# Kernel optimization log

Measured on AMD Instinct MI355X. Metric: run time of the kernel, lower is better.

The kernel has to match this reference:

```python
import jax, jax.numpy as jnp
import numpy as np

N_NODES = 100000
N_EDGES = 1600000
D_IN = 128
D_HID = 64
N_CLASSES = 64


def setup_inputs() -> dict:
    key = jax.random.key(0)
    ks = jax.random.split(key, 12)
    x = jax.random.normal(ks[0], (N_NODES, D_IN), dtype=jnp.float32)
    edge_index = jax.random.randint(ks[1], (2, N_EDGES), 0, N_NODES, dtype=jnp.int64)
    def lin(k, fan_in, fan_out):
        k1, k2 = jax.random.split(k)
        bound = 1.0 / np.sqrt(fan_in)
        w = jax.random.uniform(k1, (fan_in, fan_out), jnp.float32, -bound, bound)
        b = jax.random.uniform(k2, (fan_out,), jnp.float32, -bound, bound)
        return w, b
    w1a, b1a = lin(ks[2], D_IN, D_HID)
    w1b, b1b = lin(ks[3], D_HID, D_HID)
    w2a, b2a = lin(ks[4], D_HID, D_HID)
    w2b, b2b = lin(ks[5], D_HID, N_CLASSES)
    return {"x": x, "edge_index": edge_index,
            "w1a": w1a, "b1a": b1a, "w1b": w1b, "b1b": b1b,
            "w2a": w2a, "b2a": b2a, "w2b": w2b, "b2b": b2b}


def _gin_agg(x, src, dst):
    # GINConv with eps=0: (1+eps)*x_i + sum_{j->i} x_j
    agg = jax.ops.segment_sum(x[src], dst, num_segments=N_NODES)
    return x + agg


def reference(x, edge_index, w1a, b1a, w1b, b1b, w2a, b2a, w2b, b2b):
    src, dst = edge_index[0], edge_index[1]
    # conv1: MLP = Linear -> ReLU -> Linear -> ReLU
    h = _gin_agg(x, src, dst)
    h = jax.nn.relu(h @ w1a + b1a)
    h = jax.nn.relu(h @ w1b + b1b)
    # conv2: MLP = Linear -> ReLU -> Linear
    h = _gin_agg(h, src, dst)
    h = jax.nn.relu(h @ w2a + b2a)
    h = h @ w2b + b2b
    # global add pool over the single graph -> [1, num_classes]
    return jnp.sum(h, axis=0, keepdims=True)
```

## Files before the change

kernel.cpp:

```cpp
#include <hip/hip_runtime.h>

#define N_NODES 100000
#define N_EDGES 1600000
#define D_IN 128
#define D 64

#define NBLK 1000
#define EPB  1600
#define NB2  391
#define SC_M  (NB2 * NBLK)
#define SC_CH 1024
#define SC_NB ((SC_M + SC_CH - 1) / SC_CH)

__device__ __forceinline__ float bf2f(unsigned short u) {
    union { unsigned int i; float f; } q; q.i = ((unsigned int)u) << 16; return q.f;
}
__device__ __forceinline__ unsigned short f2bf(float f) {
    unsigned int u = __float_as_uint(f);
    unsigned int r = (u + 0x7FFFu + ((u >> 16) & 1u)) >> 16;
    return (unsigned short)r;
}
__device__ __forceinline__ void acc4(float4& a, ushort4 v) {
    a.x += bf2f(v.x); a.y += bf2f(v.y); a.z += bf2f(v.z); a.w += bf2f(v.w);
}


__global__ __launch_bounds__(256) void k_hist1(const int* __restrict__ dst,
                                               int* __restrict__ bh) {
    __shared__ int h[NB2];
    int t = threadIdx.x;
    for (int i = t; i < NB2; i += 256) h[i] = 0;
    __syncthreads();
    int base = blockIdx.x * EPB;
    for (int i = t; i < EPB; i += 256) atomicAdd(&h[dst[base + i] >> 8], 1);
    __syncthreads();
    for (int i = t; i < NB2; i += 256) bh[i * NBLK + blockIdx.x] = h[i];
}

__global__ __launch_bounds__(256) void k_scanA(const int* __restrict__ bh,
                                               int* __restrict__ part) {
    __shared__ int s[256];
    int t = threadIdx.x;
    int base = blockIdx.x * SC_CH + t * 4;
    int sum = 0;
    if (base + 3 < SC_M) {
        int4 v = *(const int4*)(bh + base);
        sum = (v.x + v.y) + (v.z + v.w);
    } else {
        for (int k = 0; k < 4; k++) if (base + k < SC_M) sum += bh[base + k];
    }
    s[t] = sum;
    __syncthreads();
    for (int o = 128; o > 0; o >>= 1) {
        if (t < o) s[t] += s[t + o];
        __syncthreads();
    }
    if (t == 0) part[blockIdx.x] = s[0];
}

__global__ __launch_bounds__(512) void k_scanB(int* __restrict__ part) {
    __shared__ int s[512];
    int t = threadIdx.x;
    int v = (t < SC_NB) ? part[t] : 0;
    s[t] = v;
    __syncthreads();
    for (int o = 1; o < 512; o <<= 1) {
        int x = (t >= o) ? s[t - o] : 0;
        __syncthreads();
        s[t] += x;
        __syncthreads();
    }
    if (t < SC_NB) part[t] = s[t] - v;
}

__global__ __launch_bounds__(256) void k_scanC(int* __restrict__ bh,
                                               const int* __restrict__ part) {
    __shared__ int s[256];
    int t = threadIdx.x;
    int base = blockIdx.x * SC_CH + t * 4;
    int4 v = {0, 0, 0, 0};
    if (base + 3 < SC_M) v = *(const int4*)(bh + base);
    else { for (int k = 0; k < 4; k++) if (base + k < SC_M) (&v.x)[k] = bh[base + k]; }
    int sum = (v.x + v.y) + (v.z + v.w);
    s[t] = sum;
    __syncthreads();
    for (int o = 1; o < 256; o <<= 1) {
        int x = (t >= o) ? s[t - o] : 0;
        __syncthreads();
        s[t] += x;
        __syncthreads();
    }
    int run = part[blockIdx.x] + s[t] - sum;
    int4 w;
    w.x = run; run += v.x;
    w.y = run; run += v.y;
    w.z = run; run += v.z;
    w.w = run;
    if (base + 3 < SC_M) *(int4*)(bh + base) = w;
    else { for (int k = 0; k < 4; k++) if (base + k < SC_M) bh[base + k] = (&w.x)[k]; }
}

__global__ __launch_bounds__(256) void k_scatter1(const int* __restrict__ src,
                                                  const int* __restrict__ dst,
                                                  const int* __restrict__ bh,
                                                  uint2* __restrict__ tmp) {
    __shared__ int cur[NB2];
    int t = threadIdx.x;
    for (int i = t; i < NB2; i += 256) cur[i] = bh[i * NBLK + blockIdx.x];
    __syncthreads();
    int base = blockIdx.x * EPB;
    for (int i = t; i < EPB; i += 256) {
        int d = dst[base + i];
        int sv = src[base + i];
        int p = atomicAdd(&cur[d >> 8], 1);
        tmp[p] = make_uint2((unsigned)d, (unsigned)sv);
    }
}

__global__ __launch_bounds__(256) void k_build(const uint2* __restrict__ tmp,
                                               const int* __restrict__ bh,
                                               int* __restrict__ offs,
                                               int* __restrict__ csr) {
    __shared__ int deg[256];
    __shared__ int s[256];
    __shared__ int cur[256];
    int b = blockIdx.x;
    int t = threadIdx.x;
    int e0 = bh[b * NBLK];
    int e1 = (b == NB2 - 1) ? N_EDGES : bh[(b + 1) * NBLK];
    deg[t] = 0;
    __syncthreads();
    for (int i = e0 + t; i < e1; i += 256) atomicAdd(&deg[tmp[i].x & 255u], 1);
    __syncthreads();
    int v = deg[t];
    s[t] = v;
    __syncthreads();
    for (int o = 1; o < 256; o <<= 1) {
        int x = (t >= o) ? s[t - o] : 0;
        __syncthreads();
        s[t] += x;
        __syncthreads();
    }
    int start = e0 + s[t] - v;
    int node = b * 256 + t;
    if (node < N_NODES) offs[node] = start;
    cur[t] = start;
    __syncthreads();
    for (int i = e0 + t; i < e1; i += 256) {
        uint2 p = tmp[i];
        int pos = atomicAdd(&cur[p.x & 255u], 1);
        csr[pos] = (int)p.y;
    }
    if (b == 0 && t == 0) offs[N_NODES] = N_EDGES;
}

__global__ __launch_bounds__(256) void k_gemm1(const float* __restrict__ x,
                                               const float* __restrict__ w,
                                               unsigned short* __restrict__ z) {
    __shared__ float ws[D_IN][D];
    __shared__ float xs[16][D_IN + 1];
    int t = threadIdx.x;
    {
        const float4* w4 = (const float4*)w;
        float4* s4 = (float4*)&ws[0][0];
        for (int i = t; i < (D_IN * D) / 4; i += 256) s4[i] = w4[i];
    }
    int r = t >> 4, c = t & 15;
    __syncthreads();
    for (int base = blockIdx.x * 16; base < N_NODES; base += gridDim.x * 16) {
        for (int i = t; i < 16 * (D_IN / 4); i += 256) {
            int row = i >> 5, k4 = i & 31;
            float4 v = ((const float4*)(x + (size_t)(base + row) * D_IN))[k4];
            xs[row][k4 * 4 + 0] = v.x; xs[row][k4 * 4 + 1] = v.y;
            xs[row][k4 * 4 + 2] = v.z; xs[row][k4 * 4 + 3] = v.w;
        }
        __syncthreads();
        float4 acc = {0.f, 0.f, 0.f, 0.f};
        for (int k = 0; k < D_IN; k++) {
            float xv = xs[r][k];
            float4 wv = *(const float4*)&ws[k][c * 4];
            acc.x += xv * wv.x; acc.y += xv * wv.y;
            acc.z += xv * wv.z; acc.w += xv * wv.w;
        }
        ushort4 p;
        p.x = f2bf(acc.x); p.y = f2bf(acc.y); p.z = f2bf(acc.z); p.w = f2bf(acc.w);
        *(ushort4*)(z + (size_t)(base + r) * D + c * 4) = p;
        __syncthreads();
    }
}

__device__ __forceinline__ void gather16(float4& acc, const unsigned short* __restrict__ zz,
                                         const int* __restrict__ csr,
                                         int e0, int e1, size_t c4) {
    for (int e = e0; e < e1; e += 16) {
        int idx[16];
        #pragma unroll
        for (int k = 0; k < 16; k++) {
            int ee = e + k;
            idx[k] = csr[ee < e1 ? ee : e1 - 1];
        }
        ushort4 vv[16];
        #pragma unroll
        for (int k = 0; k < 16; k++)
            vv[k] = *(const ushort4*)(zz + (size_t)idx[k] * D + c4);
        #pragma unroll
        for (int k = 0; k < 16; k++) {
            if (e + k < e1) acc4(acc, vv[k]);
        }
    }
}

__global__ __launch_bounds__(256, 6) void k_conv1(const unsigned short* __restrict__ z,
                                                  const int* __restrict__ offs,
                                                  const int* __restrict__ csr,
                                                  const float* __restrict__ b1a,
                                                  const float* __restrict__ w1b,
                                                  const float* __restrict__ b1b,
                                                  const float* __restrict__ w2a,
                                                  unsigned short* __restrict__ u) {
    __shared__ unsigned short w1s[D][D];
    __shared__ unsigned short w2s[D][D];
    __shared__ float h1s[16][D + 1];
    __shared__ float h2s[16][D + 1];
    int t = threadIdx.x;
    int r = t >> 4, c = t & 15;
    {
        for (int i = t; i < (D * D) / 4; i += 256) {
            float4 a = ((const float4*)w1b)[i];
            ushort4 p; p.x = f2bf(a.x); p.y = f2bf(a.y); p.z = f2bf(a.z); p.w = f2bf(a.w);
            *(ushort4*)&(&w1s[0][0])[i * 4] = p;
            float4 b = ((const float4*)w2a)[i];
            ushort4 q; q.x = f2bf(b.x); q.y = f2bf(b.y); q.z = f2bf(b.z); q.w = f2bf(b.w);
            *(ushort4*)&(&w2s[0][0])[i * 4] = q;
        }
    }
    float4 vb1a = ((const float4*)b1a)[c];
    float4 vb1b = ((const float4*)b1b)[c];
    __syncthreads();

    const size_t c4 = (size_t)(c * 4);
    for (int base = blockIdx.x * 16; base < N_NODES; base += gridDim.x * 16) {
        int node = base + r;
        float4 acc = {vb1a.x, vb1a.y, vb1a.z, vb1a.w};
        acc4(acc, *(const ushort4*)(z + (size_t)node * D + c4));
        int e0 = offs[node], e1 = offs[node + 1];
        gather16(acc, z, csr, e0, e1, c4);
        h1s[r][c * 4 + 0] = fmaxf(acc.x, 0.f);
        h1s[r][c * 4 + 1] = fmaxf(acc.y, 0.f);
        h1s[r][c * 4 + 2] = fmaxf(acc.z, 0.f);
        h1s[r][c * 4 + 3] = fmaxf(acc.w, 0.f);
        __syncthreads();
        float4 a2 = vb1b;
        for (int k = 0; k < D; k++) {
            float hv = h1s[r][k];
            ushort4 wv = *(const ushort4*)&w1s[k][c * 4];
            a2.x += hv * bf2f(wv.x); a2.y += hv * bf2f(wv.y);
            a2.z += hv * bf2f(wv.z); a2.w += hv * bf2f(wv.w);
        }
        h2s[r][c * 4 + 0] = fmaxf(a2.x, 0.f);
        h2s[r][c * 4 + 1] = fmaxf(a2.y, 0.f);
        h2s[r][c * 4 + 2] = fmaxf(a2.z, 0.f);
        h2s[r][c * 4 + 3] = fmaxf(a2.w, 0.f);
        __syncthreads();
        float4 a3 = {0.f, 0.f, 0.f, 0.f};
        for (int k = 0; k < D; k++) {
            float hv = h2s[r][k];
            ushort4 wv = *(const ushort4*)&w2s[k][c * 4];
            a3.x += hv * bf2f(wv.x); a3.y += hv * bf2f(wv.y);
            a3.z += hv * bf2f(wv.z); a3.w += hv * bf2f(wv.w);
        }
        ushort4 p;
        p.x = f2bf(a3.x); p.y = f2bf(a3.y); p.z = f2bf(a3.z); p.w = f2bf(a3.w);
        *(ushort4*)(u + (size_t)node * D + c4) = p;
        __syncthreads();
    }
}

__global__ __launch_bounds__(256) void k_conv2(const unsigned short* __restrict__ u,
                                               const int* __restrict__ offs,
                                               const int* __restrict__ csr,
                                               const float* __restrict__ b2a,
                                               float* __restrict__ colsum) {
    __shared__ float red[16][D + 1];
    int t = threadIdx.x;
    int r = t >> 4, c = t & 15;
    float4 vb = ((const float4*)b2a)[c];
    float4 cs = {0.f, 0.f, 0.f, 0.f};
    const size_t c4 = (size_t)(c * 4);
    for (int base = blockIdx.x * 16; base < N_NODES; base += gridDim.x * 16) {
        int node = base + r;
        float4 acc = {vb.x, vb.y, vb.z, vb.w};
        acc4(acc, *(const ushort4*)(u + (size_t)node * D + c4));
        int e0 = offs[node], e1 = offs[node + 1];
        gather16(acc, u, csr, e0, e1, c4);
        cs.x += fmaxf(acc.x, 0.f); cs.y += fmaxf(acc.y, 0.f);
        cs.z += fmaxf(acc.z, 0.f); cs.w += fmaxf(acc.w, 0.f);
    }
    red[r][c * 4 + 0] = cs.x; red[r][c * 4 + 1] = cs.y;
    red[r][c * 4 + 2] = cs.z; red[r][c * 4 + 3] = cs.w;
    __syncthreads();
    if (r == 0) {
        float4 tot = {0.f, 0.f, 0.f, 0.f};
        for (int rr = 0; rr < 16; rr++) {
            tot.x += red[rr][c * 4 + 0]; tot.y += red[rr][c * 4 + 1];
            tot.z += red[rr][c * 4 + 2]; tot.w += red[rr][c * 4 + 3];
        }
        atomicAdd(&colsum[c * 4 + 0], tot.x);
        atomicAdd(&colsum[c * 4 + 1], tot.y);
        atomicAdd(&colsum[c * 4 + 2], tot.z);
        atomicAdd(&colsum[c * 4 + 3], tot.w);
    }
}

__global__ void k_final(const float* __restrict__ colsum, const float* __restrict__ w2b,
                        const float* __restrict__ b2b, float* __restrict__ out) {
    int j = threadIdx.x;
    float acc = (float)N_NODES * b2b[j];
    for (int k = 0; k < D; k++) acc += colsum[k] * w2b[k * D + j];
    out[j] = acc;
}


extern "C" void kernel_launch(void* const* d_in, const int* in_sizes, int n_in,
                              void* d_out, int out_size, void* d_ws, size_t ws_size,
                              hipStream_t stream) {
    const float* x   = (const float*)d_in[0];
    const int*   ei  = (const int*)d_in[1];
    const float* w1a = (const float*)d_in[2];
    const float* b1a = (const float*)d_in[3];
    const float* w1b = (const float*)d_in[4];
    const float* b1b = (const float*)d_in[5];
    const float* w2a = (const float*)d_in[6];
    const float* b2a = (const float*)d_in[7];
    const float* w2b = (const float*)d_in[8];
    const float* b2b = (const float*)d_in[9];
    float* out = (float*)d_out;

    const int* srcp = ei;
    const int* dstp = ei + N_EDGES;

    char* ws = (char*)d_ws;
    unsigned short* z = (unsigned short*)(ws + 0);
    unsigned short* u = (unsigned short*)(ws + 12800000);
    uint2* tmp    = (uint2*)(ws + 25600000);
    int*   csr    = (int*)(ws + 38400000);
    int*   bh     = (int*)(ws + 44800000);
    int*   offs   = (int*)(ws + 46364000);
    float* colsum = (float*)(ws + 46764032);
    int*   part   = (int*)(ws + 46764288);

    hipMemsetAsync(colsum, 0, D * sizeof(float), stream);

    k_hist1   <<<NBLK, 256, 0, stream>>>(dstp, bh);
    k_scanA   <<<SC_NB, 256, 0, stream>>>(bh, part);
    k_scanB   <<<1, 512, 0, stream>>>(part);
    k_scanC   <<<SC_NB, 256, 0, stream>>>(bh, part);
    k_scatter1<<<NBLK, 256, 0, stream>>>(srcp, dstp, bh, tmp);
    k_build   <<<NB2, 256, 0, stream>>>(tmp, bh, offs, csr);

    k_gemm1<<<2048, 256, 0, stream>>>(x, w1a, z);
    k_conv1<<<2048, 256, 0, stream>>>(z, offs, csr, b1a, w1b, b1b, w2a, u);
    k_conv2<<<2048, 256, 0, stream>>>(u, offs, csr, b2a, colsum);
    k_final<<<1, 64, 0, stream>>>(colsum, w2b, b2b, out);
}
```

Baseline: 492.9 us.

## Pad CSR neighbor lists to multiples of 16 with a zero dummy node

Builds a padded CSR in which each node's neighbor list is rounded up to a multiple of 16 and the padding points to an extra zero row at index N_NODES. The gather loop can then use aligned int4 index loads with no bounds clamping or predication. This needs two extra kernels (per-block padded sums and a scan) plus memsets for the dummy rows. The cost is more wasted gathers, since with an average degree of 16 the padding adds roughly half as many dummy loads again.

```diff
diff --git a/kernel.cpp b/kernel.cpp
--- a/kernel.cpp
+++ b/kernel.cpp
@@ -117,23 +117,63 @@
     }
 }
 
-__global__ __launch_bounds__(256) void k_build(const uint2* __restrict__ tmp,
-                                               const int* __restrict__ bh,
-                                               int* __restrict__ offs,
-                                               int* __restrict__ csr) {
+__global__ __launch_bounds__(256) void k_padsum(const uint2* __restrict__ tmp,
+                                                const int* __restrict__ bh,
+                                                int* __restrict__ degarr,
+                                                int* __restrict__ pb) {
     __shared__ int deg[256];
     __shared__ int s[256];
-    __shared__ int cur[256];
-    int b = blockIdx.x;
-    int t = threadIdx.x;
+    int b = blockIdx.x, t = threadIdx.x;
     int e0 = bh[b * NBLK];
     int e1 = (b == NB2 - 1) ? N_EDGES : bh[(b + 1) * NBLK];
     deg[t] = 0;
     __syncthreads();
     for (int i = e0 + t; i < e1; i += 256) atomicAdd(&deg[tmp[i].x & 255u], 1);
     __syncthreads();
-    int v = deg[t];
+    int node = b * 256 + t;
+    int d = (node < N_NODES) ? deg[t] : 0;
+    if (node < N_NODES) degarr[node] = d;
+    int dp = (d + 15) & ~15;
+    s[t] = dp;
+    __syncthreads();
+    for (int o = 128; o > 0; o >>= 1) {
+        if (t < o) s[t] += s[t + o];
+        __syncthreads();
+    }
+    if (t == 0) pb[b] = s[0];
+}
+
+__global__ __launch_bounds__(512) void k_scanP(int* __restrict__ pb) {
+    __shared__ int s[512];
+    int t = threadIdx.x;
+    int v = (t < NB2) ? pb[t] : 0;
     s[t] = v;
+    __syncthreads();
+    for (int o = 1; o < 512; o <<= 1) {
+        int x = (t >= o) ? s[t - o] : 0;
+        __syncthreads();
+        s[t] += x;
+        __syncthreads();
+    }
+    if (t < NB2) pb[t] = s[t] - v;
+}
+
+__global__ __launch_bounds__(256) void k_build2(const uint2* __restrict__ tmp,
+                                                const int* __restrict__ bh,
+                                                const int* __restrict__ degarr,
+                                                const int* __restrict__ pb,
+                                                int* __restrict__ offs,
+                                                int* __restrict__ csr) {
+    __shared__ int s[256];
+    __shared__ int startp[256];
+    __shared__ int cur[256];
+    int b = blockIdx.x, t = threadIdx.x;
+    int e0 = bh[b * NBLK];
+    int e1 = (b == NB2 - 1) ? N_EDGES : bh[(b + 1) * NBLK];
+    int node = b * 256 + t;
+    int d = (node < N_NODES) ? degarr[node] : 0;
+    int dp = (d + 15) & ~15;
+    s[t] = dp;
     __syncthreads();
     for (int o = 1; o < 256; o <<= 1) {
         int x = (t >= o) ? s[t - o] : 0;
@@ -141,17 +181,22 @@
         s[t] += x;
         __syncthreads();
     }
-    int start = e0 + s[t] - v;
-    int node = b * 256 + t;
-    if (node < N_NODES) offs[node] = start;
-    cur[t] = start;
+    int st = pb[b] + s[t] - dp;
+    startp[t] = st;
+    cur[t] = st;
+    if (node < N_NODES) {
+        offs[node] = st;
+        if (node == N_NODES - 1) offs[N_NODES] = st + dp;
+    }
     __syncthreads();
     for (int i = e0 + t; i < e1; i += 256) {
         uint2 p = tmp[i];
         int pos = atomicAdd(&cur[p.x & 255u], 1);
         csr[pos] = (int)p.y;
     }
-    if (b == 0 && t == 0) offs[N_NODES] = N_EDGES;
+    __syncthreads();
+    int end = startp[t] + dp;
+    for (int p = cur[t]; p < end; p++) csr[p] = N_NODES;
 }
 
 __global__ __launch_bounds__(256) void k_gemm1(const float* __restrict__ x,
@@ -189,24 +234,21 @@
     }
 }
 
-__device__ __forceinline__ void gather16(float4& acc, const unsigned short* __restrict__ zz,
-                                         const int* __restrict__ csr,
-                                         int e0, int e1, size_t c4) {
+__device__ __forceinline__ void gather16p(float4& acc, const unsigned short* __restrict__ zz,
+                                          const int* __restrict__ csr,
+                                          int e0, int e1, size_t c4) {
     for (int e = e0; e < e1; e += 16) {
         int idx[16];
-        #pragma unroll
-        for (int k = 0; k < 16; k++) {
-            int ee = e + k;
-            idx[k] = csr[ee < e1 ? ee : e1 - 1];
-        }
+        *(int4*)(&idx[0])  = *(const int4*)(csr + e);
+        *(int4*)(&idx[4])  = *(const int4*)(csr + e + 4);
+        *(int4*)(&idx[8])  = *(const int4*)(csr + e + 8);
+        *(int4*)(&idx[12]) = *(const int4*)(csr + e + 12);
         ushort4 vv[16];
         #pragma unroll
         for (int k = 0; k < 16; k++)
             vv[k] = *(const ushort4*)(zz + (size_t)idx[k] * D + c4);
         #pragma unroll
-        for (int k = 0; k < 16; k++) {
-            if (e + k < e1) acc4(acc, vv[k]);
-        }
+        for (int k = 0; k < 16; k++) acc4(acc, vv[k]);
     }
 }
 
@@ -244,7 +286,7 @@
         float4 acc = {vb1a.x, vb1a.y, vb1a.z, vb1a.w};
         acc4(acc, *(const ushort4*)(z + (size_t)node * D + c4));
         int e0 = offs[node], e1 = offs[node + 1];
-        gather16(acc, z, csr, e0, e1, c4);
+        gather16p(acc, z, csr, e0, e1, c4);
         h1s[r][c * 4 + 0] = fmaxf(acc.x, 0.f);
         h1s[r][c * 4 + 1] = fmaxf(acc.y, 0.f);
         h1s[r][c * 4 + 2] = fmaxf(acc.z, 0.f);
@@ -292,7 +334,7 @@
         float4 acc = {vb.x, vb.y, vb.z, vb.w};
         acc4(acc, *(const ushort4*)(u + (size_t)node * D + c4));
         int e0 = offs[node], e1 = offs[node + 1];
-        gather16(acc, u, csr, e0, e1, c4);
+        gather16p(acc, u, csr, e0, e1, c4);
         cs.x += fmaxf(acc.x, 0.f); cs.y += fmaxf(acc.y, 0.f);
         cs.z += fmaxf(acc.z, 0.f); cs.w += fmaxf(acc.w, 0.f);
     }
@@ -341,22 +383,28 @@
 
     char* ws = (char*)d_ws;
     unsigned short* z = (unsigned short*)(ws + 0);
-    unsigned short* u = (unsigned short*)(ws + 12800000);
-    uint2* tmp    = (uint2*)(ws + 25600000);
-    int*   csr    = (int*)(ws + 38400000);
-    int*   bh     = (int*)(ws + 44800000);
-    int*   offs   = (int*)(ws + 46364000);
-    float* colsum = (float*)(ws + 46764032);
-    int*   part   = (int*)(ws + 46764288);
+    unsigned short* u = (unsigned short*)(ws + 12800256);
+    uint2* tmp    = (uint2*)(ws + 25600512);
+    int*   csr    = (int*)(ws + 38400512);
+    int*   bh     = (int*)(ws + 51200512);
+    int*   degarr = (int*)(ws + 52764512);
+    int*   offs   = (int*)(ws + 53164896);
+    int*   pb     = (int*)(ws + 53564960);
+    int*   part   = (int*)(ws + 53567008);
+    float* colsum = (float*)(ws + 53569056);
 
     hipMemsetAsync(colsum, 0, D * sizeof(float), stream);
+    hipMemsetAsync(z + (size_t)N_NODES * D, 0, D * sizeof(unsigned short), stream);
+    hipMemsetAsync(u + (size_t)N_NODES * D, 0, D * sizeof(unsigned short), stream);
 
     k_hist1   <<<NBLK, 256, 0, stream>>>(dstp, bh);
     k_scanA   <<<SC_NB, 256, 0, stream>>>(bh, part);
     k_scanB   <<<1, 512, 0, stream>>>(part);
     k_scanC   <<<SC_NB, 256, 0, stream>>>(bh, part);
     k_scatter1<<<NBLK, 256, 0, stream>>>(srcp, dstp, bh, tmp);
-    k_build   <<<NB2, 256, 0, stream>>>(tmp, bh, offs, csr);
+    k_padsum  <<<NB2, 256, 0, stream>>>(tmp, bh, degarr, pb);
+    k_scanP   <<<1, 512, 0, stream>>>(pb);
+    k_build2  <<<NB2, 256, 0, stream>>>(tmp, bh, degarr, pb, offs, csr);
 
     k_gemm1<<<2048, 256, 0, stream>>>(x, w1a, z);
     k_conv1<<<2048, 256, 0, stream>>>(z, offs, csr, b1a, w1b, b1b, w2a, u);
```

After: 485.3 us. No clear change (-1.5%).
